# Kernel optimization log

Hardware: AMD Instinct MI355X
Metric: run time of the kernel (lower is better)

## Reference

```python
import math
import jax, jax.numpy as jnp
import numpy as np

N_HEAD = 16
NUM_BUCKETS = 32
MAX_DISTANCE = 2048
NEG_INF = -1e9  # finite stand-in for -inf in masked_fill; rows always have >=1 unmasked entry


def _relative_position_bucket(relative_position, num_buckets=NUM_BUCKETS, max_distance=MAX_DISTANCE):
    # causal (bidirectional=False) T5 bucketing
    rp = -jnp.minimum(relative_position, 0)  # nonneg distances
    max_exact = num_buckets // 2
    is_small = rp < max_exact
    rp_safe = jnp.maximum(rp, 1).astype(jnp.float32)
    large = max_exact + (
        jnp.log(rp_safe / max_exact) / math.log(max_distance / max_exact) * (num_buckets - max_exact)
    ).astype(jnp.int32)
    large = jnp.minimum(large, num_buckets - 1)
    return jnp.where(is_small, rp, large)


def t5_bias(rel_table, T):
    ctx = jnp.arange(T)[:, None]
    mem = jnp.arange(T)[None, :]
    buckets = _relative_position_bucket(mem - ctx)        # [T, T]
    bias = rel_table[buckets]                              # [T, T, H]
    return jnp.transpose(bias, (2, 0, 1))                  # [H, T, T]


def setup_inputs() -> dict:
    key = jax.random.key(0)
    k1, k2, k3, k4 = jax.random.split(key, 4)
    B, T, C = 2, 2048, 1024
    x = jax.random.normal(k1, (B, T, C), dtype=jnp.float32)
    w_qkv = jax.random.normal(k2, (C, 3 * C), dtype=jnp.float32) * (1.0 / math.sqrt(C))
    w_proj = jax.random.normal(k3, (C, C), dtype=jnp.float32) * (1.0 / math.sqrt(C))
    rel_table = jax.random.normal(k4, (NUM_BUCKETS, N_HEAD), dtype=jnp.float32) * 0.02
    return {"x": x, "w_qkv": w_qkv, "w_proj": w_proj, "rel_table": rel_table}


def reference(x, w_qkv, w_proj, rel_table):
    B, T, C = x.shape
    H = N_HEAD
    d = C // H
    qkv = x @ w_qkv                                        # [B, T, 3C]
    q, k, v = jnp.split(qkv, 3, axis=-1)
    q = q.reshape(B, T, H, d).transpose(0, 2, 1, 3)        # [B, H, T, d]
    k = k.reshape(B, T, H, d).transpose(0, 2, 1, 3)
    v = v.reshape(B, T, H, d).transpose(0, 2, 1, 3)

    bias = t5_bias(rel_table, T)                           # [H, T, T]
    causal = jnp.tril(jnp.ones((T, T), dtype=bool))
    bias = jnp.where(causal[None], bias, NEG_INF)          # masked_fill(-inf) on bias

    scores = jnp.einsum("bhqd,bhkd->bhqk", q, k) * (1.0 / math.sqrt(d))
    scores = scores + bias[None]                           # broadcast over batch
    att = jax.nn.softmax(scores, axis=-1)
    y = jnp.einsum("bhqk,bhkd->bhqd", att, v)              # [B, H, T, d]
    y = y.transpose(0, 2, 1, 3).reshape(B, T, C)
    return y @ w_proj
```

## Files before the change

### kernel.cpp

```cpp
#include <hip/hip_runtime.h>
#include <hip/hip_bf16.h>
#include <cstdint>
#include <cstddef>

#define B_  2
#define T_  2048
#define C_  1024
#define H_  16
#define D_  64
#define NEG_INF_ -1e9f

typedef short bf16x8 __attribute__((ext_vector_type(8)));
typedef float f32x4  __attribute__((ext_vector_type(4)));

__device__ __forceinline__ short f2bf(float f) {
  union { float f; unsigned u; } x; x.f = f;
  unsigned r = (x.u + 0x7fffu + ((x.u >> 16) & 1u)) >> 16;
  return (short)r;
}

__device__ __forceinline__ void gload16(const void* g, void* l) {
  __builtin_amdgcn_global_load_lds(
      (const __attribute__((address_space(1))) unsigned int*)g,
      (__attribute__((address_space(3))) unsigned int*)l, 16, 0, 0);
}

__global__ __launch_bounds__(256) void cvt_bf16(const float* __restrict__ in,
                                                short* __restrict__ out, int n4) {
  int i = blockIdx.x * 256 + threadIdx.x;
  if (i < n4) {
    float4 v = ((const float4*)in)[i];
    short4 o;
    o.x = f2bf(v.x); o.y = f2bf(v.y); o.z = f2bf(v.z); o.w = f2bf(v.w);
    ((short4*)out)[i] = o;
  }
}

__global__ __launch_bounds__(256) void transpose_cvt(const float* __restrict__ in,
                                                     short* __restrict__ out,
                                                     int R, int C) {
  __shared__ float tile[32][33];
  int gx = blockIdx.x * 32, gy = blockIdx.y * 32;
  int tx = threadIdx.x, ty = threadIdx.y;
#pragma unroll
  for (int i = 0; i < 4; ++i)
    tile[ty + i * 8][tx] = in[(size_t)(gy + ty + i * 8) * C + gx + tx];
  __syncthreads();
#pragma unroll
  for (int i = 0; i < 4; ++i)
    out[(size_t)(gx + ty + i * 8) * R + gy + tx] = f2bf(tile[tx][ty + i * 8]);
}

__global__ __launch_bounds__(256) void bias_table(const float* __restrict__ rel_table,
                                                  float* __restrict__ btab) {
  int idx = blockIdx.x * 256 + threadIdx.x;
  if (idx >= H_ * T_) return;
  int dist = idx & (T_ - 1);
  int h = idx >> 11;
  int bucket;
  if (dist < 16) {
    bucket = dist;
  } else {
    float rp = (float)dist;
    int large = 16 + (int)(logf(rp * (1.0f / 16.0f)) * (1.0f / logf(128.0f)) * 16.0f);
    bucket = large < 31 ? large : 31;
  }
  btab[idx] = rel_table[bucket * H_ + h];
}

template <int MODE>
__global__ __launch_bounds__(256) void gemm_bt128(
    const short* __restrict__ A, const short* __restrict__ Bt,
    int M, int N, int K,
    short* __restrict__ q_out, short* __restrict__ k_out,
    short* __restrict__ vT_out, float* __restrict__ f_out) {
  __shared__ alignas(16) short As[128 * 64];
  __shared__ alignas(16) short Bs[128 * 64];
  const int tid = threadIdx.x;
  const int w = tid >> 6, lane = tid & 63;
  const int g = lane >> 4, l16 = lane & 15;
  const int wr = w >> 1, wc = w & 1;
  const int m0 = blockIdx.y * 128, n0 = blockIdx.x * 128;

  const char* Ag = (const char*)(A + (size_t)m0 * K);
  const char* Bg = (const char*)(Bt + (size_t)n0 * K);
  char* AsB = (char*)As;
  char* BsB = (char*)Bs;

  int goff[4];
#pragma unroll
  for (int i = 0; i < 4; ++i) {
    int o = i * 256 + tid;
    int row = o >> 3, ch = o & 7;
    goff[i] = row * (K * 2) + ((ch ^ (row & 7)) << 4);
  }

  f32x4 acc[4][4] = {};

  const int nkt = K >> 6;
  for (int kt = 0; kt < nkt; ++kt) {
    __syncthreads();
    const int kbyte = kt << 7;
#pragma unroll
    for (int i = 0; i < 4; ++i)
      gload16(Ag + goff[i] + kbyte, AsB + i * 4096 + w * 1024);
#pragma unroll
    for (int i = 0; i < 4; ++i)
      gload16(Bg + goff[i] + kbyte, BsB + i * 4096 + w * 1024);
    __syncthreads();
#pragma unroll
    for (int kk = 0; kk < 2; ++kk) {
      bf16x8 af[4], bff[4];
#pragma unroll
      for (int m = 0; m < 4; ++m) {
        int r = wr * 64 + m * 16 + l16;
        int off = (r * 128 + kk * 64 + g * 16) ^ ((r & 7) << 4);
        af[m] = *(const bf16x8*)(AsB + off);
      }
#pragma unroll
      for (int n = 0; n < 4; ++n) {
        int c = wc * 64 + n * 16 + l16;
        int off = (c * 128 + kk * 64 + g * 16) ^ ((c & 7) << 4);
        bff[n] = *(const bf16x8*)(BsB + off);
      }
#pragma unroll
      for (int m = 0; m < 4; ++m)
#pragma unroll
        for (int n = 0; n < 4; ++n)
          acc[m][n] = __builtin_amdgcn_mfma_f32_16x16x32_bf16(af[m], bff[n], acc[m][n], 0, 0, 0);
    }
  }

#pragma unroll
  for (int m = 0; m < 4; ++m) {
#pragma unroll
    for (int n = 0; n < 4; ++n) {
      const int colg = n0 + wc * 64 + n * 16 + l16;
#pragma unroll
      for (int r = 0; r < 4; ++r) {
        const int rowg = m0 + wr * 64 + m * 16 + g * 4 + r;
        float v = acc[m][n][r];
        if (MODE == 1) {
          f_out[(size_t)rowg * N + colg] = v;
        } else {
          int part = colg >> 10;
          int within = colg & 1023;
          int h = within >> 6, dd = within & 63;
          int b = rowg >> 11, t = rowg & (T_ - 1);
          size_t bh = (size_t)(b * H_ + h);
          if (part == 0)
            q_out[(bh * T_ + t) * D_ + dd] = f2bf(v * 0.125f);
          else if (part == 1)
            k_out[(bh * T_ + t) * D_ + dd] = f2bf(v);
          else
            vT_out[(bh * D_ + dd) * T_ + t] = f2bf(v);
        }
      }
    }
  }
}

__global__ __launch_bounds__(256) void attn64(
    const short* __restrict__ qb, const short* __restrict__ kb,
    const short* __restrict__ vTb, const float* __restrict__ bias_tab,
    short* __restrict__ yb) {
  __shared__ alignas(16) short Ks[2][64 * 64];
  __shared__ alignas(16) short Vs[2][64 * 64];
  __shared__ alignas(16) short Ps[4][16 * 64];
  __shared__ float biasw[2][2][128];
  const int tid = threadIdx.x;
  const int w = tid >> 6, lane = tid & 63;
  const int g = lane >> 4, l16 = lane & 15;
  const int bh = blockIdx.y;
  const int h = bh & (H_ - 1);
  const int b = bh >> 4;
  const int j = blockIdx.x;
  const int qlo = j, qhi = 31 - j;
  const int q0l = qlo * 64, q0h = qhi * 64;

  const char* kbase = (const char*)(kb + (size_t)bh * T_ * D_);
  const char* vbase = (const char*)(vTb + (size_t)bh * D_ * T_);
  const float* btab = bias_tab + h * T_;

  bf16x8 qfl[2], qfh[2];
  {
    const short* qrl = qb + ((size_t)bh * T_ + q0l + w * 16 + l16) * D_;
    qfl[0] = *(const bf16x8*)(qrl + g * 8);
    qfl[1] = *(const bf16x8*)(qrl + 32 + g * 8);
    const short* qrh = qb + ((size_t)bh * T_ + q0h + w * 16 + l16) * D_;
    qfh[0] = *(const bf16x8*)(qrh + g * 8);
    qfh[1] = *(const bf16x8*)(qrh + 32 + g * 8);
  }

  f32x4 accl[4] = {}, acch[4] = {};
  float ml[4], ll[4], mh[4], lh[4];
#pragma unroll
  for (int r = 0; r < 4; ++r) { ml[r] = mh[r] = -1e30f; ll[r] = lh[r] = 0.f; }

  char* PsB = (char*)&Ps[w][0];

  int krow[2], kch[2];
#pragma unroll
  for (int i = 0; i < 2; ++i) {
    int o = i * 256 + tid;
    krow[i] = o >> 3;
    kch[i] = (o & 7) ^ (krow[i] & 7);
  }

  auto stageKV = [&](int buf, int t) {
    const int kv0 = t * 64;
    char* KsB = (char*)&Ks[buf][0];
    char* VsB = (char*)&Vs[buf][0];
#pragma unroll
    for (int i = 0; i < 2; ++i)
      gload16(kbase + (size_t)(kv0 + krow[i]) * 128 + kch[i] * 16,
              KsB + i * 4096 + w * 1024);
#pragma unroll
    for (int i = 0; i < 2; ++i)
      gload16(vbase + (size_t)krow[i] * (T_ * 2) + kv0 * 2 + kch[i] * 16,
              VsB + i * 4096 + w * 1024);
  };
  auto biasLoad = [&](int t) -> float {
    int i = tid & 127;
    int q0x = (tid >= 128) ? q0h : q0l;
    int d = q0x - t * 64 - 63 + i;
    return (d >= 0 && d < T_) ? btab[d] : NEG_INF_;
  };

  auto computeTile = [&](const char* KsB, const char* VsB, const float* bw,
                         const bf16x8* qf, f32x4* acc, float* mrun, float* lrun) {
    f32x4 s[4];
    __builtin_amdgcn_s_setprio(1);
#pragma unroll
    for (int n = 0; n < 4; ++n) {
      int kvrow = n * 16 + l16;
      int off0 = (kvrow * 128 + g * 16) ^ ((kvrow & 7) << 4);
      int off1 = (kvrow * 128 + 64 + g * 16) ^ ((kvrow & 7) << 4);
      bf16x8 k0 = *(const bf16x8*)(KsB + off0);
      bf16x8 k1 = *(const bf16x8*)(KsB + off1);
      f32x4 z = {};
      z = __builtin_amdgcn_mfma_f32_16x16x32_bf16(qf[0], k0, z, 0, 0, 0);
      z = __builtin_amdgcn_mfma_f32_16x16x32_bf16(qf[1], k1, z, 0, 0, 0);
      s[n] = z;
    }
    __builtin_amdgcn_s_setprio(0);

    float sv[4][4];
    float tmax[4] = {-1e30f, -1e30f, -1e30f, -1e30f};
#pragma unroll
    for (int n = 0; n < 4; ++n) {
#pragma unroll
      for (int r = 0; r < 4; ++r) {
        int idx = 63 + w * 16 + g * 4 + r - n * 16 - l16;
        float val = s[n][r] + bw[idx];
        sv[n][r] = val;
        tmax[r] = fmaxf(tmax[r], val);
      }
    }
#pragma unroll
    for (int r = 0; r < 4; ++r) {
      float v = tmax[r];
      v = fmaxf(v, __shfl_xor(v, 1));
      v = fmaxf(v, __shfl_xor(v, 2));
      v = fmaxf(v, __shfl_xor(v, 4));
      v = fmaxf(v, __shfl_xor(v, 8));
      tmax[r] = v;
    }

    bool nogrow = true;
#pragma unroll
    for (int r = 0; r < 4; ++r) nogrow &= (tmax[r] <= mrun[r] + 8.0f);
    if (!__all(nogrow)) {
#pragma unroll
      for (int r = 0; r < 4; ++r) {
        float mnew = fmaxf(mrun[r], tmax[r]);
        float scale = __expf(mrun[r] - mnew);
        mrun[r] = mnew;
        lrun[r] *= scale;
#pragma unroll
        for (int dn = 0; dn < 4; ++dn) acc[dn][r] *= scale;
      }
    }

#pragma unroll
    for (int r = 0; r < 4; ++r) {
      float su = 0.f;
#pragma unroll
      for (int n = 0; n < 4; ++n) {
        float p = __expf(sv[n][r] - mrun[r]);
        su += p;
        int row = g * 4 + r, col = n * 16 + l16;
        int off = (row * 128 + col * 2) ^ ((row & 7) << 4);
        *(short*)(PsB + off) = f2bf(p);
      }
      lrun[r] += su;
    }

    bf16x8 pf[2];
    {
      int o0 = (l16 * 128 + g * 16) ^ ((l16 & 7) << 4);
      int o1 = (l16 * 128 + 64 + g * 16) ^ ((l16 & 7) << 4);
      pf[0] = *(const bf16x8*)(PsB + o0);
      pf[1] = *(const bf16x8*)(PsB + o1);
    }
    __builtin_amdgcn_s_setprio(1);
#pragma unroll
    for (int dn = 0; dn < 4; ++dn) {
      int drow = dn * 16 + l16;
      int o0 = (drow * 128 + g * 16) ^ ((drow & 7) << 4);
      int o1 = (drow * 128 + 64 + g * 16) ^ ((drow & 7) << 4);
      bf16x8 v0 = *(const bf16x8*)(VsB + o0);
      bf16x8 v1 = *(const bf16x8*)(VsB + o1);
      acc[dn] = __builtin_amdgcn_mfma_f32_16x16x32_bf16(pf[0], v0, acc[dn], 0, 0, 0);
      acc[dn] = __builtin_amdgcn_mfma_f32_16x16x32_bf16(pf[1], v1, acc[dn], 0, 0, 0);
    }
    __builtin_amdgcn_s_setprio(0);
  };

  stageKV(0, 0);
  {
    float bv = biasLoad(0);
    biasw[0][tid >> 7][tid & 127] = bv;
  }
  __syncthreads();

  int cur = 0;
  for (int t = 0; t <= qhi; ++t) {
    const int nxt = cur ^ 1;
    const bool hasnext = (t < qhi);
    float bvn = 0.f;
    if (hasnext) {
      stageKV(nxt, t + 1);
      bvn = biasLoad(t + 1);
    }
    if (t <= qlo)
      computeTile((const char*)&Ks[cur][0], (const char*)&Vs[cur][0],
                  &biasw[cur][0][0], qfl, accl, ml, ll);
    computeTile((const char*)&Ks[cur][0], (const char*)&Vs[cur][0],
                &biasw[cur][1][0], qfh, acch, mh, lh);
    if (hasnext) biasw[nxt][tid >> 7][tid & 127] = bvn;
    __syncthreads();
    cur = nxt;
  }

  auto writeO = [&](int q0x, const f32x4* acc, float* lrun) {
#pragma unroll
    for (int r = 0; r < 4; ++r) {
      float v = lrun[r];
      v += __shfl_xor(v, 1);
      v += __shfl_xor(v, 2);
      v += __shfl_xor(v, 4);
      v += __shfl_xor(v, 8);
      float inv = 1.0f / v;
      int qg = q0x + w * 16 + g * 4 + r;
      size_t ybase = ((size_t)b * T_ + qg) * C_ + h * D_;
#pragma unroll
      for (int dn = 0; dn < 4; ++dn)
        yb[ybase + dn * 16 + l16] = f2bf(acc[dn][r] * inv);
    }
  };
  writeO(q0l, accl, ll);
  writeO(q0h, acch, lh);
}

extern "C" void kernel_launch(void* const* d_in, const int* in_sizes, int n_in,
                              void* d_out, int out_size, void* d_ws, size_t ws_size,
                              hipStream_t stream) {
  const float* x = (const float*)d_in[0];
  const float* w_qkv = (const float*)d_in[1];
  const float* w_proj = (const float*)d_in[2];
  const float* rel_table = (const float*)d_in[3];
  float* out = (float*)d_out;

  const size_t MB = 1024 * 1024;
  char* ws = (char*)d_ws;
  short* xb     = (short*)(ws);
  short* wqkvT  = (short*)(ws + 8 * MB);
  short* wprojT = (short*)(ws + 14 * MB);
  short* qb     = (short*)(ws + 16 * MB);
  short* kbuf   = (short*)(ws + 24 * MB);
  short* vT     = (short*)(ws + 32 * MB);
  short* yb     = (short*)(ws + 40 * MB);
  float* btab   = (float*)(ws + 48 * MB);

  cvt_bf16<<<4096, 256, 0, stream>>>(x, xb, (B_ * T_ * C_) / 4);
  dim3 tb(32, 8);
  transpose_cvt<<<dim3(96, 32), tb, 0, stream>>>(w_qkv, wqkvT, 1024, 3072);
  transpose_cvt<<<dim3(32, 32), tb, 0, stream>>>(w_proj, wprojT, 1024, 1024);
  bias_table<<<128, 256, 0, stream>>>(rel_table, btab);

  gemm_bt128<0><<<dim3(24, 32), 256, 0, stream>>>(xb, wqkvT, 4096, 3072, 1024,
                                                  qb, kbuf, vT, nullptr);
  attn64<<<dim3(16, 32), 256, 0, stream>>>(qb, kbuf, vT, btab, yb);

  gemm_bt128<1><<<dim3(8, 32), 256, 0, stream>>>(yb, wprojT, 4096, 1024, 1024,
                                                 nullptr, nullptr, nullptr, out);
}
```

Baseline: 224.8 us.

## Split attention KV range across two blocks and merge partial softmax results

The attention grid gains a z dimension of two. Each block processes alternating KV tiles and writes unnormalized partial outputs plus running max and sum, and a new merge kernel combines the two partials with log-sum-exp weights. V staging is now single-buffered and issued just before it is needed, with an explicit vmcnt wait and barrier placed between softmax and the PV MFMA. This doubles the number of blocks to improve CU occupancy on the 512-block grid. The cost is an extra kernel launch, extra global traffic for the partials, and bf16 rounding of the unnormalized partials. The partial buffers reuse workspace regions (xb, and space past the weights) that are no longer needed at that point.

```diff
diff --git a/kernel.cpp b/kernel.cpp
--- a/kernel.cpp
+++ b/kernel.cpp
@@ -17,6 +17,12 @@
   union { float f; unsigned u; } x; x.f = f;
   unsigned r = (x.u + 0x7fffu + ((x.u >> 16) & 1u)) >> 16;
   return (short)r;
+}
+
+__device__ __forceinline__ float bf2f(short s) {
+  union { float f; unsigned u; } x;
+  x.u = ((unsigned)(unsigned short)s) << 16;
+  return x.f;
 }
 
 __device__ __forceinline__ void gload16(const void* g, void* l) {
@@ -163,9 +169,9 @@
 __global__ __launch_bounds__(256) void attn64(
     const short* __restrict__ qb, const short* __restrict__ kb,
     const short* __restrict__ vTb, const float* __restrict__ bias_tab,
-    short* __restrict__ yb) {
+    short* __restrict__ o1, short* __restrict__ o2, float* __restrict__ mlb) {
   __shared__ alignas(16) short Ks[2][64 * 64];
-  __shared__ alignas(16) short Vs[2][64 * 64];
+  __shared__ alignas(16) short Vs[64 * 64];
   __shared__ alignas(16) short Ps[4][16 * 64];
   __shared__ float biasw[2][2][128];
   const int tid = threadIdx.x;
@@ -175,6 +181,7 @@
   const int h = bh & (H_ - 1);
   const int b = bh >> 4;
   const int j = blockIdx.x;
+  const int s = blockIdx.z;
   const int qlo = j, qhi = 31 - j;
   const int q0l = qlo * 64, q0h = qhi * 64;
 
@@ -193,9 +200,9 @@
   }
 
   f32x4 accl[4] = {}, acch[4] = {};
-  float ml[4], ll[4], mh[4], lh[4];
-#pragma unroll
-  for (int r = 0; r < 4; ++r) { ml[r] = mh[r] = -1e30f; ll[r] = lh[r] = 0.f; }
+  float mlo[4], llo[4], mhi[4], lhi[4];
+#pragma unroll
+  for (int r = 0; r < 4; ++r) { mlo[r] = mhi[r] = -1e30f; llo[r] = lhi[r] = 0.f; }
 
   char* PsB = (char*)&Ps[w][0];
 
@@ -207,14 +214,17 @@
     kch[i] = (o & 7) ^ (krow[i] & 7);
   }
 
-  auto stageKV = [&](int buf, int t) {
+  auto stageK = [&](int buf, int t) {
     const int kv0 = t * 64;
     char* KsB = (char*)&Ks[buf][0];
-    char* VsB = (char*)&Vs[buf][0];
 #pragma unroll
     for (int i = 0; i < 2; ++i)
       gload16(kbase + (size_t)(kv0 + krow[i]) * 128 + kch[i] * 16,
               KsB + i * 4096 + w * 1024);
+  };
+  auto stageV = [&](int t) {
+    const int kv0 = t * 64;
+    char* VsB = (char*)Vs;
 #pragma unroll
     for (int i = 0; i < 2; ++i)
       gload16(vbase + (size_t)krow[i] * (T_ * 2) + kv0 * 2 + kch[i] * 16,
@@ -227,9 +237,10 @@
     return (d >= 0 && d < T_) ? btab[d] : NEG_INF_;
   };
 
-  auto computeTile = [&](const char* KsB, const char* VsB, const float* bw,
-                         const bf16x8* qf, f32x4* acc, float* mrun, float* lrun) {
-    f32x4 s[4];
+  auto computeTile = [&](const char* KsB, const float* bw, const bf16x8* qf,
+                         f32x4* acc, float* mrun, float* lrun,
+                         bool dosync, bool drain2) {
+    f32x4 sreg[4];
     __builtin_amdgcn_s_setprio(1);
 #pragma unroll
     for (int n = 0; n < 4; ++n) {
@@ -241,7 +252,7 @@
       f32x4 z = {};
       z = __builtin_amdgcn_mfma_f32_16x16x32_bf16(qf[0], k0, z, 0, 0, 0);
       z = __builtin_amdgcn_mfma_f32_16x16x32_bf16(qf[1], k1, z, 0, 0, 0);
-      s[n] = z;
+      sreg[n] = z;
     }
     __builtin_amdgcn_s_setprio(0);
 
@@ -252,7 +263,7 @@
 #pragma unroll
       for (int r = 0; r < 4; ++r) {
         int idx = 63 + w * 16 + g * 4 + r - n * 16 - l16;
-        float val = s[n][r] + bw[idx];
+        float val = sreg[n][r] + bw[idx];
         sv[n][r] = val;
         tmax[r] = fmaxf(tmax[r], val);
       }
@@ -296,6 +307,17 @@
       lrun[r] += su;
     }
 
+    if (dosync) {
+      if (drain2) {
+        asm volatile("s_waitcnt vmcnt(2)" ::: "memory");
+      } else {
+        asm volatile("s_waitcnt vmcnt(0)" ::: "memory");
+      }
+      __builtin_amdgcn_s_barrier();
+      __builtin_amdgcn_sched_barrier(0);
+    }
+
+    const char* VsB = (const char*)Vs;
     bf16x8 pf[2];
     {
       int o0 = (l16 * 128 + g * 16) ^ ((l16 & 7) << 4);
@@ -317,33 +339,35 @@
     __builtin_amdgcn_s_setprio(0);
   };
 
-  stageKV(0, 0);
+  stageK(0, s);
   {
-    float bv = biasLoad(0);
+    float bv = biasLoad(s);
     biasw[0][tid >> 7][tid & 127] = bv;
   }
   __syncthreads();
 
   int cur = 0;
-  for (int t = 0; t <= qhi; ++t) {
+  for (int t = s; t <= qhi; t += 2) {
     const int nxt = cur ^ 1;
-    const bool hasnext = (t < qhi);
+    const bool hasnext = (t + 2 <= qhi);
     float bvn = 0.f;
-    if (hasnext) {
-      stageKV(nxt, t + 1);
-      bvn = biasLoad(t + 1);
-    }
-    if (t <= qlo)
-      computeTile((const char*)&Ks[cur][0], (const char*)&Vs[cur][0],
-                  &biasw[cur][0][0], qfl, accl, ml, ll);
-    computeTile((const char*)&Ks[cur][0], (const char*)&Vs[cur][0],
-                &biasw[cur][1][0], qfh, acch, mh, lh);
+    if (hasnext) bvn = biasLoad(t + 2);
+    stageV(t);
+    if (hasnext) stageK(nxt, t + 2);
+    const char* KsB = (const char*)&Ks[cur][0];
+    bool first = true;
+    if (t <= qlo) {
+      computeTile(KsB, &biasw[cur][0][0], qfl, accl, mlo, llo, true, hasnext);
+      first = false;
+    }
+    computeTile(KsB, &biasw[cur][1][0], qfh, acch, mhi, lhi, first, hasnext);
     if (hasnext) biasw[nxt][tid >> 7][tid & 127] = bvn;
     __syncthreads();
     cur = nxt;
   }
 
-  auto writeO = [&](int q0x, const f32x4* acc, float* lrun) {
+  short* dst = (s == 0) ? o1 : o2;
+  auto writeO = [&](int q0x, const f32x4* acc, const float* mrun, float* lrun) {
 #pragma unroll
     for (int r = 0; r < 4; ++r) {
       float v = lrun[r];
@@ -351,16 +375,39 @@
       v += __shfl_xor(v, 2);
       v += __shfl_xor(v, 4);
       v += __shfl_xor(v, 8);
-      float inv = 1.0f / v;
       int qg = q0x + w * 16 + g * 4 + r;
       size_t ybase = ((size_t)b * T_ + qg) * C_ + h * D_;
 #pragma unroll
       for (int dn = 0; dn < 4; ++dn)
-        yb[ybase + dn * 16 + l16] = f2bf(acc[dn][r] * inv);
+        dst[ybase + dn * 16 + l16] = f2bf(acc[dn][r]);
+      if (l16 == 0) {
+        int idx = (((b * T_) + qg) * H_ + h) * 4 + s * 2;
+        mlb[idx] = mrun[r];
+        mlb[idx + 1] = v;
+      }
     }
   };
-  writeO(q0l, accl, ll);
-  writeO(q0h, acch, lh);
+  writeO(q0l, accl, mlo, llo);
+  writeO(q0h, acch, mhi, lhi);
+}
+
+__global__ __launch_bounds__(256) void attn_merge(
+    short* __restrict__ o1, const short* __restrict__ o2,
+    const float* __restrict__ mlb) {
+  int i = blockIdx.x * 256 + threadIdx.x;
+  int row = i >> 7;
+  int h = (i & 127) >> 3;
+  float4 q = ((const float4*)mlb)[row * H_ + h];
+  float m = fmaxf(q.x, q.z);
+  float w0 = __expf(q.x - m), w1 = __expf(q.z - m);
+  float inv = 1.0f / (w0 * q.y + w1 * q.w);
+  bf16x8 a = ((const bf16x8*)o1)[i];
+  bf16x8 bb = ((const bf16x8*)o2)[i];
+  bf16x8 o;
+#pragma unroll
+  for (int e = 0; e < 8; ++e)
+    o[e] = f2bf((w0 * bf2f(a[e]) + w1 * bf2f(bb[e])) * inv);
+  ((bf16x8*)o1)[i] = o;
 }
 
 extern "C" void kernel_launch(void* const* d_in, const int* in_sizes, int n_in,
@@ -382,6 +429,8 @@
   short* vT     = (short*)(ws + 32 * MB);
   short* yb     = (short*)(ws + 40 * MB);
   float* btab   = (float*)(ws + 48 * MB);
+  short* o2b    = (short*)(ws);
+  float* mlb    = (float*)(ws + 9 * MB);
 
   cvt_bf16<<<4096, 256, 0, stream>>>(x, xb, (B_ * T_ * C_) / 4);
   dim3 tb(32, 8);
@@ -391,7 +440,8 @@
 
   gemm_bt128<0><<<dim3(24, 32), 256, 0, stream>>>(xb, wqkvT, 4096, 3072, 1024,
                                                   qb, kbuf, vT, nullptr);
-  attn64<<<dim3(16, 32), 256, 0, stream>>>(qb, kbuf, vT, btab, yb);
+  attn64<<<dim3(16, 32, 2), 256, 0, stream>>>(qb, kbuf, vT, btab, yb, o2b, mlb);
+  attn_merge<<<2048, 256, 0, stream>>>(yb, o2b, mlb);
 
   gemm_bt128<1><<<dim3(8, 32), 256, 0, stream>>>(yb, wprojT, 4096, 1024, 1024,
                                                  nullptr, nullptr, nullptr, out);
```

Measured after the change: 227.0 us. About the same (+1.0%).
